# Performance work log

Measured on AMD Instinct MI355X. Metric: run time of the kernel, lower is better.

Reference implementation:

```python
import jax, jax.numpy as jnp
import numpy as np

N, E, D_IN, D_OUT = 50000, 600000, 128, 128
BETA, ALPHA = 0.4, 0.6


def setup_inputs() -> dict:
    key = jax.random.key(0)
    ks = jax.random.split(key, 8)
    def xavier(k, shape):
        std = (2.0 / (shape[0] + shape[1])) ** 0.5
        return jax.random.normal(k, shape, jnp.float32) * std
    x = jax.random.normal(ks[0], (N, D_IN), jnp.float32)
    edge_index = jax.random.randint(ks[1], (2, E), 0, N, jnp.int32)
    Wq = xavier(ks[2], (D_IN, D_OUT))
    Wk = xavier(ks[3], (D_IN, D_OUT))
    Wv = xavier(ks[4], (D_IN, D_IN))
    W_gcn = xavier(ks[5], (D_IN, D_IN))   # GCNConv linear weight [out, in]
    b_gcn = jnp.zeros((D_IN,), jnp.float32)
    W_lin = xavier(ks[6], (D_OUT, D_IN))  # nn.Linear weight [out, in]
    b_lin = jnp.zeros((D_OUT,), jnp.float32)
    return {"x": x, "edge_index": edge_index, "Wq": Wq, "Wk": Wk, "Wv": Wv,
            "W_gcn": W_gcn, "b_gcn": b_gcn, "W_lin": W_lin, "b_lin": b_lin}


def gcn_conv(x, edge_index, W, b):
    # PyG GCNConv default: add self-loops, symmetric deg^-1/2 normalization.
    n = x.shape[0]
    loops = jnp.arange(n, dtype=edge_index.dtype)
    src = jnp.concatenate([edge_index[0], loops])
    dst = jnp.concatenate([edge_index[1], loops])
    deg = jax.ops.segment_sum(jnp.ones_like(dst, jnp.float32), dst, num_segments=n)
    d_inv_sqrt = jax.lax.rsqrt(deg)  # deg >= 1 thanks to self-loops
    norm = d_inv_sqrt[src] * d_inv_sqrt[dst]  # [E+N]
    xw = x @ W.T                               # [N, d]
    out = jax.ops.segment_sum(xw[src] * norm[:, None], dst, num_segments=n)
    return out + b


def reference(x, edge_index, Wq, Wk, Wv, W_gcn, b_gcn, W_lin, b_lin):
    n, d_in = x.shape
    q = x @ Wq
    q_hat = q / jnp.linalg.norm(q)  # Frobenius norm
    k = x @ Wk
    k_hat = k / jnp.linalg.norm(k)
    v = x @ Wv
    # qk = q_hat @ (k_hat^T @ 1) / in_channels  -> [n]
    qk = (q_hat @ k_hat.sum(axis=0)) / d_in
    # D = diag(1 + qk); inverse of diagonal is elementwise reciprocal
    scale = 1.0 / (1.0 + qk)
    attn = v + (q_hat @ (k_hat.T @ v)) / d_in  # [n, d_in]
    Z = BETA * scale[:, None] * attn + (1.0 - BETA) * x
    gcn = gcn_conv(x, edge_index, W_gcn, b_gcn)
    # self.dropout(gcn) result is discarded in the source -> no-op
    Z_out = (1.0 - ALPHA) * Z + ALPHA * gcn
    return Z_out @ W_lin.T + b_lin
```

## Files before the change

kernel.cpp:

```cpp
#include <hip/hip_runtime.h>
#include <hip/hip_fp16.h>
#include <cstdint>
#include <cstddef>

#define D 128
typedef unsigned short u16;
typedef short bf16x8 __attribute__((ext_vector_type(8)));
typedef float f32x4 __attribute__((ext_vector_type(4)));

__device__ __forceinline__ u16 f2b(float f) {
    uint32_t u = __float_as_uint(f);
    return (u16)((u + 0x7FFFu + ((u >> 16) & 1u)) >> 16);
}
__device__ __forceinline__ float b2f(u16 b) {
    return __uint_as_float(((uint32_t)b) << 16);
}

#define SWZ(r, k) ((k) ^ (((r) & 7) << 3))

__global__ void k_prep(const float* __restrict__ Wq, const float* __restrict__ Wk,
                       const float* __restrict__ Wv, const float* __restrict__ Wg,
                       const float* __restrict__ bg, const float* __restrict__ Wl,
                       const float* __restrict__ bl,
                       u16* __restrict__ Bcatb, float* __restrict__ biasout)
{
    const int b = blockIdx.x;
    const int t = threadIdx.x;
    if (b < 640) {
        const int strip = b >> 7, n = b & 127;
        float val;
        if (strip == 0) {
            val = Wq[t * D + n];
        } else if (strip == 1) {
            val = Wk[t * D + n];
        } else if (strip == 2) {
            float s = 0.f;
#pragma unroll 8
            for (int m = 0; m < D; ++m) s += Wv[t * D + m] * Wl[n * D + m];
            val = s;
        } else if (strip == 3) {
            val = Wl[n * D + t];
        } else {
            float s = 0.f;
#pragma unroll 8
            for (int m = 0; m < D; ++m) s += Wl[n * D + m] * Wg[m * D + t];
            val = 0.6f * s;
        }
        Bcatb[(size_t)b * D + t] = f2b(val);
    } else {
        float s = 0.f;
#pragma unroll 8
        for (int m = 0; m < D; ++m) s += bg[m] * Wl[t * D + m];
        biasout[t] = bl[t] + 0.6f * s;
    }
}

__global__ void k_init(int* __restrict__ cnt, int M)
{
    const int i = blockIdx.x * 256 + threadIdx.x;
    if (i < M) cnt[i] = 0;
}

__global__ void k_hist(const int* __restrict__ dst, int* __restrict__ cnt,
                       int* __restrict__ epos, int E)
{
    const int e = blockIdx.x * 256 + threadIdx.x;
    if (e < E) epos[e] = atomicAdd(&cnt[dst[e]], 1);
}

__global__ __launch_bounds__(1024) void k_scan1(const int* __restrict__ cnt,
                                                int* __restrict__ offs,
                                                int* __restrict__ bsum,
                                                float* __restrict__ dinv, int M)
{
    __shared__ int wsum[16];
    const int t = threadIdx.x, lane = t & 63, w = t >> 6;
    const int i = blockIdx.x * 1024 + t;
    const int v = (i < M) ? cnt[i] : 0;
    if (i < M) dinv[i] = rsqrtf((float)(v + 1));
    int s = v;
    for (int off = 1; off < 64; off <<= 1) {
        int n = __shfl_up(s, off);
        if (lane >= off) s += n;
    }
    if (lane == 63) wsum[w] = s;
    __syncthreads();
    if (w == 0) {
        int ss = (lane < 16) ? wsum[lane] : 0;
        for (int off = 1; off < 16; off <<= 1) {
            int n = __shfl_up(ss, off);
            if (lane >= off) ss += n;
        }
        if (lane < 16) wsum[lane] = ss;
    }
    __syncthreads();
    const int woff = (w == 0) ? 0 : wsum[w - 1];
    if (i < M) offs[i] = woff + s - v;
    if (t == 1023) bsum[blockIdx.x] = wsum[15];
}

__global__ void k_scanB(int* __restrict__ bsum, int nb)
{
    const int t = threadIdx.x;
    int v = (t < nb) ? bsum[t] : 0;
    int s = v;
    for (int off = 1; off < 64; off <<= 1) {
        int n = __shfl_up(s, off);
        if (t >= off) s += n;
    }
    if (t < nb) bsum[t] = s - v;
}

__global__ void k_scan2(const int* __restrict__ bsum, int* __restrict__ offs, int M)
{
    const int i = blockIdx.x * 256 + threadIdx.x;
    if (i < M) offs[i] += bsum[i >> 10];
}

__global__ void k_fill(const int* __restrict__ src, const int* __restrict__ dst,
                       const int* __restrict__ epos,
                       const float* __restrict__ dinv,
                       const int* __restrict__ offs,
                       uint32_t* __restrict__ cpk, int E)
{
    const int e = blockIdx.x * 256 + threadIdx.x;
    if (e < E) {
        const int s = src[e], d = dst[e];
        const int pos = offs[d] + epos[e];
        const float w = dinv[s] * dinv[d];
        const u16 hb = __half_as_ushort(__float2half(w));
        cpk[pos] = (uint32_t)(u16)s | ((uint32_t)hb << 16);
    }
}

__global__ __launch_bounds__(256) void k_gemm5(const float* __restrict__ x,
                                               const u16* __restrict__ Bcatb,
                                               u16* __restrict__ outbase,
                                               float* __restrict__ psq,
                                               float* __restrict__ psk,
                                               float* __restrict__ pks,
                                               int M, size_t NQ)
{
    __shared__ u16 As[64 * D];
    __shared__ u16 Bs[64 * D];
    __shared__ float lks[D];
    __shared__ float red[4];
    const int t = threadIdx.x;
    const int row0 = blockIdx.x * 64;
    const int pair = blockIdx.y;

    if (t < D) lks[t] = 0.f;

#pragma unroll
    for (int p = 0; p < 4; ++p) {
        const int flat = t + 256 * p;
        const int r = flat >> 4, kg = flat & 15;
        int gr = row0 + r; if (gr > M - 1) gr = M - 1;
        const float4 f0 = *(const float4*)(x + (size_t)gr * D + kg * 8);
        const float4 f1 = *(const float4*)(x + (size_t)gr * D + kg * 8 + 4);
        u16 rr[8] = {f2b(f0.x), f2b(f0.y), f2b(f0.z), f2b(f0.w),
                     f2b(f1.x), f2b(f1.y), f2b(f1.z), f2b(f1.w)};
        *(uint4*)(As + r * D + SWZ(r, kg * 8)) = *(const uint4*)rr;
    }
#pragma unroll
    for (int p = 0; p < 4; ++p) {
        const int flat = t + 256 * p;
        const int r = flat >> 4, kg = flat & 15;
        const uint4 v = *(const uint4*)(Bcatb + (size_t)(2 * pair * 64 + r) * D + kg * 8);
        *(uint4*)(Bs + r * D + SWZ(r, kg * 8)) = v;
    }
    __syncthreads();

    const int lane = t & 63, w = t >> 6;
    const int wr = (w >> 1) * 32, wc = (w & 1) * 32;
    const int fr = lane & 15, kg2 = lane >> 4;

    u16* outp = outbase + (size_t)pair * NQ;
    float sacc = 0.f;
    float kc[4] = {0.f, 0.f, 0.f, 0.f};

#pragma unroll
    for (int h = 0; h < 2; ++h) {
        f32x4 acc[2][2] = {};
#pragma unroll
        for (int ks = 0; ks < 4; ++ks) {
            const int kb = ks * 32 + kg2 * 8;
            bf16x8 a[2], b[2];
#pragma unroll
            for (int i = 0; i < 2; ++i) {
                const int r = wr + 16 * i + fr;
                a[i] = *(const bf16x8*)(As + r * D + SWZ(r, kb));
            }
#pragma unroll
            for (int j = 0; j < 2; ++j) {
                const int r = wc + 16 * j + fr;
                b[j] = *(const bf16x8*)(Bs + r * D + SWZ(r, kb));
            }
#pragma unroll
            for (int i = 0; i < 2; ++i)
#pragma unroll
                for (int j = 0; j < 2; ++j)
                    acc[i][j] = __builtin_amdgcn_mfma_f32_16x16x32_bf16(a[i], b[j], acc[i][j], 0, 0, 0);
        }
        __syncthreads();
        if (h == 0) {
#pragma unroll
            for (int p = 0; p < 4; ++p) {
                const int flat = t + 256 * p;
                const int r = flat >> 4, kg = flat & 15;
                const uint4 v = *(const uint4*)(Bcatb + (size_t)((2 * pair + 1) * 64 + r) * D + kg * 8);
                *(uint4*)(Bs + r * D + SWZ(r, kg * 8)) = v;
            }
        }

        const int col0 = h * 64;
#pragma unroll
        for (int i = 0; i < 2; ++i) {
#pragma unroll
            for (int reg = 0; reg < 4; ++reg) {
                const int r = row0 + wr + 16 * i + kg2 * 4 + reg;
                if (r < M) {
#pragma unroll
                    for (int j = 0; j < 2; ++j) {
                        const int col = col0 + wc + 16 * j + fr;
                        const u16 hv = f2b(acc[i][j][reg]);
                        outp[(size_t)r * D + col] = hv;
                        if (pair < 2) {
                            const float v = b2f(hv);
                            sacc += v * v;
                            if (pair == 1) kc[h * 2 + j] += v;
                        }
                    }
                }
            }
        }
        if (h == 0) __syncthreads();
    }

    if (pair < 2) {
        if (pair == 1) {
#pragma unroll
            for (int h = 0; h < 2; ++h)
#pragma unroll
                for (int j = 0; j < 2; ++j)
                    atomicAdd(&lks[h * 64 + wc + 16 * j + fr], kc[h * 2 + j]);
        }
        for (int off = 32; off > 0; off >>= 1) sacc += __shfl_down(sacc, off);
        if ((t & 63) == 0) red[w] = sacc;
        __syncthreads();
        if (t == 0) {
            const float s = red[0] + red[1] + red[2] + red[3];
            if (pair == 0) psq[blockIdx.x] = s; else psk[blockIdx.x] = s;
        }
        if (pair == 1 && t < D) pks[(size_t)blockIdx.x * D + t] = lks[t];
    }
}

__global__ __launch_bounds__(256) void k_ktv(const u16* __restrict__ kb,
                                             const u16* __restrict__ vWb,
                                             float* __restrict__ part, int M)
{
    __shared__ u16 kT[D * 64];
    __shared__ u16 vT[D * 64];
    const int t = threadIdx.x;
    const int P = (int)gridDim.x;
    const int chunk = (M + P - 1) / P;
    const int rbeg = blockIdx.x * chunk;
    const int rend = min(rbeg + chunk, M);

    const int lane = t & 63, w = t >> 6;
    const int fr = lane & 15, kg = lane >> 4;

    f32x4 acc[2][8] = {};

    for (int r0 = rbeg; r0 < rend; r0 += 64) {
#pragma unroll
        for (int p = 0; p < 4; ++p) {
            const int flat = t + 256 * p;
            const int rr = flat & 63, cg = flat >> 6;
            const int gr = r0 + rr;
            uint4 kv = make_uint4(0, 0, 0, 0), vv = make_uint4(0, 0, 0, 0);
            if (gr < rend) {
                kv = *(const uint4*)(kb + (size_t)gr * D + cg * 8);
                vv = *(const uint4*)(vWb + (size_t)gr * D + cg * 8);
            }
            const u16* kp = (const u16*)&kv;
            const u16* vp = (const u16*)&vv;
#pragma unroll
            for (int jj = 0; jj < 8; ++jj) {
                const int c = cg * 8 + jj;
                const int ri = rr ^ ((c & 7) << 3);
                kT[c * 64 + ri] = kp[jj];
                vT[c * 64 + ri] = vp[jj];
            }
        }
        __syncthreads();
#pragma unroll
        for (int ks = 0; ks < 2; ++ks) {
            const int rb = ks * 32 + kg * 8;
            bf16x8 a[2], b[8];
#pragma unroll
            for (int i = 0; i < 2; ++i) {
                const int m = w * 32 + 16 * i + fr;
                a[i] = *(const bf16x8*)(kT + m * 64 + (rb ^ ((m & 7) << 3)));
            }
#pragma unroll
            for (int j = 0; j < 8; ++j) {
                const int n = 16 * j + fr;
                b[j] = *(const bf16x8*)(vT + n * 64 + (rb ^ ((n & 7) << 3)));
            }
#pragma unroll
            for (int i = 0; i < 2; ++i)
#pragma unroll
                for (int j = 0; j < 8; ++j)
                    acc[i][j] = __builtin_amdgcn_mfma_f32_16x16x32_bf16(a[i], b[j], acc[i][j], 0, 0, 0);
        }
        __syncthreads();
    }
    float* pp = part + (size_t)blockIdx.x * (D * D);
#pragma unroll
    for (int i = 0; i < 2; ++i)
#pragma unroll
        for (int reg = 0; reg < 4; ++reg) {
            const int m = w * 32 + 16 * i + kg * 4 + reg;
#pragma unroll
            for (int j = 0; j < 8; ++j)
                pp[(size_t)m * D + 16 * j + fr] = acc[i][j][reg];
        }
}

__global__ void k_redC(const float* __restrict__ part, float* __restrict__ Craw, int P)
{
    const int e = blockIdx.x * 256 + threadIdx.x;
    float s0 = 0.f, s1 = 0.f, s2 = 0.f, s3 = 0.f,
          s4 = 0.f, s5 = 0.f, s6 = 0.f, s7 = 0.f;
    int p = 0;
    for (; p + 8 <= P; p += 8) {
        s0 += part[(size_t)(p + 0) * (D * D) + e];
        s1 += part[(size_t)(p + 1) * (D * D) + e];
        s2 += part[(size_t)(p + 2) * (D * D) + e];
        s3 += part[(size_t)(p + 3) * (D * D) + e];
        s4 += part[(size_t)(p + 4) * (D * D) + e];
        s5 += part[(size_t)(p + 5) * (D * D) + e];
        s6 += part[(size_t)(p + 6) * (D * D) + e];
        s7 += part[(size_t)(p + 7) * (D * D) + e];
    }
    for (; p < P; ++p) s0 += part[(size_t)p * (D * D) + e];
    Craw[e] = ((s0 + s1) + (s2 + s3)) + ((s4 + s5) + (s6 + s7));
}

__global__ __launch_bounds__(1024) void k_scalc3t(const float* __restrict__ psq,
                                                  const float* __restrict__ psk,
                                                  const float* __restrict__ pks,
                                                  const float* __restrict__ Craw,
                                                  float* __restrict__ kq,
                                                  u16* __restrict__ C3b, int NBLK)
{
    __shared__ float lpart[8][D];
    __shared__ float wredA[16];
    __shared__ float wredB[16];
    __shared__ float invS;
    const int t = threadIdx.x;
    const int col = t & 127, grp = t >> 7;
    float s = 0.f;
#pragma unroll 8
    for (int bq = grp; bq < NBLK; bq += 8) s += pks[(size_t)bq * D + col];
    lpart[grp][col] = s;
    const int w = t >> 6, lane = t & 63;
    float a = 0.f, b = 0.f;
    for (int i = t; i < NBLK; i += 1024) { a += psq[i]; b += psk[i]; }
    for (int off = 32; off > 0; off >>= 1) {
        a += __shfl_down(a, off);
        b += __shfl_down(b, off);
    }
    if (lane == 0) { wredA[w] = a; wredB[w] = b; }
    __syncthreads();
    if (t == 0) {
        float sq = 0.f, sk = 0.f;
#pragma unroll
        for (int i = 0; i < 16; ++i) { sq += wredA[i]; sk += wredB[i]; }
        invS = 1.0f / (sqrtf(sq) * sqrtf(sk) * 128.0f);
    }
    float ks = 0.f;
    if (t < D) {
#pragma unroll
        for (int g = 0; g < 8; ++g) ks += lpart[g][t];
    }
    __syncthreads();
    const float inv = invS;
    if (t < D) kq[t] = ks * inv;
#pragma unroll
    for (int i = 0; i < 16; ++i) {
        const int e = t + 1024 * i;
        C3b[e] = f2b(Craw[(size_t)(e & 127) * D + (e >> 7)] * inv);
    }
}

__global__ __launch_bounds__(256) void k_final(const u16* __restrict__ qb,
                                               const u16* __restrict__ C3b,
                                               const u16* __restrict__ vWb,
                                               const u16* __restrict__ xWb,
                                               const u16* __restrict__ ub,
                                               const int* __restrict__ cnt,
                                               const float* __restrict__ kq,
                                               const float* __restrict__ biasout,
                                               float* __restrict__ out, int M)
{
    __shared__ u16 As[64 * D];
    __shared__ u16 Bs[D * D];
    __shared__ float scaleS[64];
    const int t = threadIdx.x;
    const int row0 = blockIdx.x * 64;

#pragma unroll
    for (int p = 0; p < 4; ++p) {
        const int flat = t + 256 * p;
        const int r = flat >> 4, kg2 = flat & 15;
        int gr = row0 + r; if (gr > M - 1) gr = M - 1;
        const uint4 v = *(const uint4*)(qb + (size_t)gr * D + kg2 * 8);
        *(uint4*)(As + r * D + SWZ(r, kg2 * 8)) = v;
    }
#pragma unroll
    for (int p = 0; p < 8; ++p) {
        const int flat = t + 256 * p;
        const int r = flat >> 4, kg2 = flat & 15;
        const uint4 v = *(const uint4*)(C3b + (size_t)r * D + kg2 * 8);
        *(uint4*)(Bs + r * D + SWZ(r, kg2 * 8)) = v;
    }
    __syncthreads();

    {
        const int rr = t >> 2, qq = t & 3;
        float s = 0.f;
#pragma unroll
        for (int i = 0; i < 4; ++i) {
            const int kk = qq * 32 + i * 8;
            const bf16x8 a = *(const bf16x8*)(As + rr * D + SWZ(rr, kk));
            const u16* ap = (const u16*)&a;
#pragma unroll
            for (int jj = 0; jj < 8; ++jj) s += b2f(ap[jj]) * kq[kk + jj];
        }
        s += __shfl_xor(s, 1);
        s += __shfl_xor(s, 2);
        if (qq == 0) scaleS[rr] = 0.16f / (1.0f + s);
    }

    const int lane = t & 63, w = t >> 6;
    const int fr = lane & 15, kg = lane >> 4;

    f32x4 acc[8] = {};
#pragma unroll
    for (int ks = 0; ks < 4; ++ks) {
        const int kb2 = ks * 32 + kg * 8;
        const int r = w * 16 + fr;
        const bf16x8 a = *(const bf16x8*)(As + r * D + SWZ(r, kb2));
#pragma unroll
        for (int j = 0; j < 8; ++j) {
            const int n = 16 * j + fr;
            const bf16x8 b = *(const bf16x8*)(Bs + n * D + SWZ(n, kb2));
            acc[j] = __builtin_amdgcn_mfma_f32_16x16x32_bf16(a, b, acc[j], 0, 0, 0);
        }
    }
    __syncthreads();

#pragma unroll
    for (int reg = 0; reg < 4; ++reg) {
        const int rr = w * 16 + kg * 4 + reg;
        const int r = row0 + rr;
        if (r < M) {
            const float rc = scaleS[rr];
            const float sc = 1.0f / (float)(cnt[r] + 1);
#pragma unroll
            for (int j = 0; j < 8; ++j) {
                const int c = 16 * j + fr;
                const size_t idx = (size_t)r * D + c;
                out[idx] = rc * (b2f(vWb[idx]) + acc[j][reg]) + 0.24f * b2f(xWb[idx])
                         + biasout[c] + sc * b2f(ub[idx]);
            }
        }
    }
}

__global__ __launch_bounds__(256) void k_gather(const int* __restrict__ offs,
                                                const int* __restrict__ cnt,
                                                const uint32_t* __restrict__ cpk,
                                                const u16* __restrict__ ub,
                                                float* __restrict__ out, int M)
{
    const int t = threadIdx.x;
    const int w = t >> 6, lane = t & 63;
    const int d = blockIdx.x * 4 + w;
    if (d >= M) return;
    const int g = lane >> 4, sub = lane & 15;
    const int beg = offs[d];
    const int n = cnt[d];
    if (n == 0) return;
    const int end = beg + n;
    float acc[8] = {};
    for (int j0 = beg; j0 < end; j0 += 8) {
        const int j1 = j0 + g, j2 = j0 + 4 + g;
        int s1 = 0, s2 = 0;
        float w1 = 0.f, w2 = 0.f;
        if (j1 < end) {
            const uint32_t p = cpk[j1];
            s1 = (int)(p & 0xFFFFu);
            w1 = __half2float(__ushort_as_half((u16)(p >> 16)));
        }
        if (j2 < end) {
            const uint32_t p = cpk[j2];
            s2 = (int)(p & 0xFFFFu);
            w2 = __half2float(__ushort_as_half((u16)(p >> 16)));
        }
        const uint4 r1 = *(const uint4*)(ub + (size_t)s1 * D + sub * 8);
        const uint4 r2 = *(const uint4*)(ub + (size_t)s2 * D + sub * 8);
        const u16* p1 = (const u16*)&r1;
        const u16* p2 = (const u16*)&r2;
#pragma unroll
        for (int i = 0; i < 8; ++i) acc[i] += w1 * b2f(p1[i]) + w2 * b2f(p2[i]);
    }
#pragma unroll
    for (int i = 0; i < 8; ++i) {
        acc[i] += __shfl_xor(acc[i], 16);
        acc[i] += __shfl_xor(acc[i], 32);
    }
    if (g == 0) {
        float* o = out + (size_t)d * D + sub * 8;
        float4 o0 = *(float4*)o, o1 = *(float4*)(o + 4);
        o0.x += acc[0]; o0.y += acc[1]; o0.z += acc[2]; o0.w += acc[3];
        o1.x += acc[4]; o1.y += acc[5]; o1.z += acc[6]; o1.w += acc[7];
        *(float4*)o = o0; *(float4*)(o + 4) = o1;
    }
}

extern "C" void kernel_launch(void* const* d_in, const int* in_sizes, int n_in,
                              void* d_out, int out_size, void* d_ws, size_t ws_size,
                              hipStream_t stream)
{
    const float* x  = (const float*)d_in[0];
    const int*   ei = (const int*)d_in[1];
    const float* Wq = (const float*)d_in[2];
    const float* Wk = (const float*)d_in[3];
    const float* Wv = (const float*)d_in[4];
    const float* Wg = (const float*)d_in[5];
    const float* bg = (const float*)d_in[6];
    const float* Wl = (const float*)d_in[7];
    const float* bl = (const float*)d_in[8];

    const int M = in_sizes[0] / D;
    const int E = in_sizes[1] / 2;
    const size_t NQ = (size_t)M * D;
    const int P = 192;
    const int NBG = (M + 63) / 64;
    const int NB = (M + 1023) / 1024;

    char* base = (char*)d_ws;
    auto alloc = [&](size_t bytes) -> char* {
        char* p = base; base += (bytes + 63) & ~(size_t)63; return p;
    };
    float* part    = (float*)alloc((size_t)P * D * D * 4);
    float* Craw    = (float*)alloc(D * D * 4);
    float* dinv    = (float*)alloc((size_t)M * 4);
    float* psq     = (float*)alloc((size_t)NBG * 4);
    float* psk     = (float*)alloc((size_t)NBG * 4);
    float* pks     = (float*)alloc((size_t)NBG * D * 4);
    float* kq      = (float*)alloc(D * 4);
    float* biasout = (float*)alloc(D * 4);
    int*   cnt     = (int*)alloc((size_t)M * 4);
    int*   offs    = (int*)alloc((size_t)M * 4);
    int*   bsum    = (int*)alloc(64 * 4);
    int*   epos    = (int*)alloc((size_t)E * 4);
    uint32_t* cpk  = (uint32_t*)alloc((size_t)E * 4);
    u16*   Bcatb   = (u16*)alloc((size_t)640 * D * 2);
    u16*   C3b     = (u16*)alloc(D * D * 2);
    u16*   qb      = (u16*)alloc(NQ * 2);
    u16*   kb      = (u16*)alloc(NQ * 2);
    u16*   vWb     = (u16*)alloc(NQ * 2);
    u16*   xWb     = (u16*)alloc(NQ * 2);
    u16*   ub      = (u16*)alloc(NQ * 2);
    (void)kb; (void)vWb; (void)xWb;

    float* out = (float*)d_out;

    k_prep<<<dim3(641), dim3(128), 0, stream>>>(Wq, Wk, Wv, Wg, bg, Wl, bl, Bcatb, biasout);
    k_init<<<(M + 255) / 256, 256, 0, stream>>>(cnt, M);
    k_hist<<<(E + 255) / 256, 256, 0, stream>>>(ei + E, cnt, epos, E);
    k_scan1<<<NB, 1024, 0, stream>>>(cnt, offs, bsum, dinv, M);
    k_scanB<<<1, 64, 0, stream>>>(bsum, NB);
    k_scan2<<<(M + 255) / 256, 256, 0, stream>>>(bsum, offs, M);
    k_fill<<<(E + 255) / 256, 256, 0, stream>>>(ei, ei + E, epos, dinv, offs, cpk, E);

    k_gemm5<<<dim3(NBG, 5), 256, 0, stream>>>(x, Bcatb, qb, psq, psk, pks, M, NQ);
    k_ktv<<<P, 256, 0, stream>>>(kb, vWb, part, M);
    k_redC<<<64, 256, 0, stream>>>(part, Craw, P);
    k_scalc3t<<<1, 1024, 0, stream>>>(psq, psk, pks, Craw, kq, C3b, NBG);

    k_final<<<(M + 63) / 64, 256, 0, stream>>>(qb, C3b, vWb, xWb, ub, cnt, kq, biasout, out, M);
    k_gather<<<(M + 3) / 4, 256, 0, stream>>>(offs, cnt, cpk, ub, out, M);
}
```

Measured before the change: 194.0 us.

## Replace per-row Q/K/V projections with Gram-matrix reformulation of linear attention

Instead of materializing q, k, vW and xW for all rows, the attention term is rewritten through the input Gram matrix X^T X and the column sums of x. This removes the large bf16 intermediates. Norms, k-sums and the q·(k^T v) product are all derived from small 128x128 matrices, computed in a single-block k_small kernel. The final kernel now recomputes from x against two weight strips per column half, and the GCN input U gets its own GEMM. This cuts global memory traffic. It adds a serial single-block stage, shared-memory atomics in the Gram kernel, and different bf16 rounding points that may change accuracy.

New measurement: 231.7 us. 19.4% more time.

```diff
diff --git a/kernel.cpp b/kernel.cpp
--- a/kernel.cpp
+++ b/kernel.cpp
@@ -18,27 +18,22 @@
 
 #define SWZ(r, k) ((k) ^ (((r) & 7) << 3))
 
-__global__ void k_prep(const float* __restrict__ Wq, const float* __restrict__ Wk,
-                       const float* __restrict__ Wv, const float* __restrict__ Wg,
+__global__ void k_prep(const float* __restrict__ Wv, const float* __restrict__ Wg,
                        const float* __restrict__ bg, const float* __restrict__ Wl,
                        const float* __restrict__ bl,
                        u16* __restrict__ Bcatb, float* __restrict__ biasout)
 {
     const int b = blockIdx.x;
     const int t = threadIdx.x;
-    if (b < 640) {
+    if (b < 384) {
         const int strip = b >> 7, n = b & 127;
         float val;
         if (strip == 0) {
-            val = Wq[t * D + n];
-        } else if (strip == 1) {
-            val = Wk[t * D + n];
-        } else if (strip == 2) {
             float s = 0.f;
 #pragma unroll 8
             for (int m = 0; m < D; ++m) s += Wv[t * D + m] * Wl[n * D + m];
             val = s;
-        } else if (strip == 3) {
+        } else if (strip == 1) {
             val = Wl[n * D + t];
         } else {
             float s = 0.f;
@@ -133,165 +128,41 @@
     }
 }
 
-__global__ __launch_bounds__(256) void k_gemm5(const float* __restrict__ x,
-                                               const u16* __restrict__ Bcatb,
-                                               u16* __restrict__ outbase,
-                                               float* __restrict__ psq,
-                                               float* __restrict__ psk,
-                                               float* __restrict__ pks,
-                                               int M, size_t NQ)
-{
-    __shared__ u16 As[64 * D];
-    __shared__ u16 Bs[64 * D];
-    __shared__ float lks[D];
-    __shared__ float red[4];
-    const int t = threadIdx.x;
-    const int row0 = blockIdx.x * 64;
-    const int pair = blockIdx.y;
-
-    if (t < D) lks[t] = 0.f;
-
-#pragma unroll
-    for (int p = 0; p < 4; ++p) {
-        const int flat = t + 256 * p;
-        const int r = flat >> 4, kg = flat & 15;
-        int gr = row0 + r; if (gr > M - 1) gr = M - 1;
-        const float4 f0 = *(const float4*)(x + (size_t)gr * D + kg * 8);
-        const float4 f1 = *(const float4*)(x + (size_t)gr * D + kg * 8 + 4);
-        u16 rr[8] = {f2b(f0.x), f2b(f0.y), f2b(f0.z), f2b(f0.w),
-                     f2b(f1.x), f2b(f1.y), f2b(f1.z), f2b(f1.w)};
-        *(uint4*)(As + r * D + SWZ(r, kg * 8)) = *(const uint4*)rr;
-    }
-#pragma unroll
-    for (int p = 0; p < 4; ++p) {
-        const int flat = t + 256 * p;
-        const int r = flat >> 4, kg = flat & 15;
-        const uint4 v = *(const uint4*)(Bcatb + (size_t)(2 * pair * 64 + r) * D + kg * 8);
-        *(uint4*)(Bs + r * D + SWZ(r, kg * 8)) = v;
-    }
-    __syncthreads();
-
-    const int lane = t & 63, w = t >> 6;
-    const int wr = (w >> 1) * 32, wc = (w & 1) * 32;
-    const int fr = lane & 15, kg2 = lane >> 4;
-
-    u16* outp = outbase + (size_t)pair * NQ;
-    float sacc = 0.f;
-    float kc[4] = {0.f, 0.f, 0.f, 0.f};
-
-#pragma unroll
-    for (int h = 0; h < 2; ++h) {
-        f32x4 acc[2][2] = {};
-#pragma unroll
-        for (int ks = 0; ks < 4; ++ks) {
-            const int kb = ks * 32 + kg2 * 8;
-            bf16x8 a[2], b[2];
-#pragma unroll
-            for (int i = 0; i < 2; ++i) {
-                const int r = wr + 16 * i + fr;
-                a[i] = *(const bf16x8*)(As + r * D + SWZ(r, kb));
-            }
-#pragma unroll
-            for (int j = 0; j < 2; ++j) {
-                const int r = wc + 16 * j + fr;
-                b[j] = *(const bf16x8*)(Bs + r * D + SWZ(r, kb));
-            }
-#pragma unroll
-            for (int i = 0; i < 2; ++i)
-#pragma unroll
-                for (int j = 0; j < 2; ++j)
-                    acc[i][j] = __builtin_amdgcn_mfma_f32_16x16x32_bf16(a[i], b[j], acc[i][j], 0, 0, 0);
-        }
-        __syncthreads();
-        if (h == 0) {
-#pragma unroll
-            for (int p = 0; p < 4; ++p) {
-                const int flat = t + 256 * p;
-                const int r = flat >> 4, kg = flat & 15;
-                const uint4 v = *(const uint4*)(Bcatb + (size_t)((2 * pair + 1) * 64 + r) * D + kg * 8);
-                *(uint4*)(Bs + r * D + SWZ(r, kg * 8)) = v;
-            }
-        }
-
-        const int col0 = h * 64;
-#pragma unroll
-        for (int i = 0; i < 2; ++i) {
-#pragma unroll
-            for (int reg = 0; reg < 4; ++reg) {
-                const int r = row0 + wr + 16 * i + kg2 * 4 + reg;
-                if (r < M) {
-#pragma unroll
-                    for (int j = 0; j < 2; ++j) {
-                        const int col = col0 + wc + 16 * j + fr;
-                        const u16 hv = f2b(acc[i][j][reg]);
-                        outp[(size_t)r * D + col] = hv;
-                        if (pair < 2) {
-                            const float v = b2f(hv);
-                            sacc += v * v;
-                            if (pair == 1) kc[h * 2 + j] += v;
-                        }
-                    }
-                }
-            }
-        }
-        if (h == 0) __syncthreads();
-    }
-
-    if (pair < 2) {
-        if (pair == 1) {
-#pragma unroll
-            for (int h = 0; h < 2; ++h)
-#pragma unroll
-                for (int j = 0; j < 2; ++j)
-                    atomicAdd(&lks[h * 64 + wc + 16 * j + fr], kc[h * 2 + j]);
-        }
-        for (int off = 32; off > 0; off >>= 1) sacc += __shfl_down(sacc, off);
-        if ((t & 63) == 0) red[w] = sacc;
-        __syncthreads();
-        if (t == 0) {
-            const float s = red[0] + red[1] + red[2] + red[3];
-            if (pair == 0) psq[blockIdx.x] = s; else psk[blockIdx.x] = s;
-        }
-        if (pair == 1 && t < D) pks[(size_t)blockIdx.x * D + t] = lks[t];
-    }
-}
-
-__global__ __launch_bounds__(256) void k_ktv(const u16* __restrict__ kb,
-                                             const u16* __restrict__ vWb,
-                                             float* __restrict__ part, int M)
-{
-    __shared__ u16 kT[D * 64];
-    __shared__ u16 vT[D * 64];
+__global__ __launch_bounds__(256) void k_gram(const float* __restrict__ x,
+                                              float* __restrict__ part,
+                                              float* __restrict__ pcs, int M)
+{
+    __shared__ u16 xT[D * 64];
+    __shared__ float lcs[D];
     const int t = threadIdx.x;
     const int P = (int)gridDim.x;
     const int chunk = (M + P - 1) / P;
     const int rbeg = blockIdx.x * chunk;
     const int rend = min(rbeg + chunk, M);
-
     const int lane = t & 63, w = t >> 6;
     const int fr = lane & 15, kg = lane >> 4;
 
+    if (t < D) lcs[t] = 0.f;
+    __syncthreads();
+
     f32x4 acc[2][8] = {};
 
     for (int r0 = rbeg; r0 < rend; r0 += 64) {
 #pragma unroll
-        for (int p = 0; p < 4; ++p) {
+        for (int p = 0; p < 8; ++p) {
             const int flat = t + 256 * p;
-            const int rr = flat & 63, cg = flat >> 6;
+            const int rr = flat >> 5;
+            const int c4 = flat & 31;
             const int gr = r0 + rr;
-            uint4 kv = make_uint4(0, 0, 0, 0), vv = make_uint4(0, 0, 0, 0);
-            if (gr < rend) {
-                kv = *(const uint4*)(kb + (size_t)gr * D + cg * 8);
-                vv = *(const uint4*)(vWb + (size_t)gr * D + cg * 8);
-            }
-            const u16* kp = (const u16*)&kv;
-            const u16* vp = (const u16*)&vv;
-#pragma unroll
-            for (int jj = 0; jj < 8; ++jj) {
-                const int c = cg * 8 + jj;
+            float4 v = make_float4(0.f, 0.f, 0.f, 0.f);
+            if (gr < rend) v = *(const float4*)(x + (size_t)gr * D + c4 * 4);
+            const float vv[4] = {v.x, v.y, v.z, v.w};
+#pragma unroll
+            for (int jj = 0; jj < 4; ++jj) {
+                const int c = c4 * 4 + jj;
                 const int ri = rr ^ ((c & 7) << 3);
-                kT[c * 64 + ri] = kp[jj];
-                vT[c * 64 + ri] = vp[jj];
+                xT[c * 64 + ri] = f2b(vv[jj]);
+                atomicAdd(&lcs[c], vv[jj]);
             }
         }
         __syncthreads();
@@ -302,12 +173,12 @@
 #pragma unroll
             for (int i = 0; i < 2; ++i) {
                 const int m = w * 32 + 16 * i + fr;
-                a[i] = *(const bf16x8*)(kT + m * 64 + (rb ^ ((m & 7) << 3)));
+                a[i] = *(const bf16x8*)(xT + m * 64 + (rb ^ ((m & 7) << 3)));
             }
 #pragma unroll
             for (int j = 0; j < 8; ++j) {
                 const int n = 16 * j + fr;
-                b[j] = *(const bf16x8*)(vT + n * 64 + (rb ^ ((n & 7) << 3)));
+                b[j] = *(const bf16x8*)(xT + n * 64 + (rb ^ ((n & 7) << 3)));
             }
 #pragma unroll
             for (int i = 0; i < 2; ++i)
@@ -327,6 +198,7 @@
             for (int j = 0; j < 8; ++j)
                 pp[(size_t)m * D + 16 * j + fr] = acc[i][j][reg];
         }
+    if (t < D) pcs[(size_t)blockIdx.x * D + t] = lcs[t];
 }
 
 __global__ void k_redC(const float* __restrict__ part, float* __restrict__ Craw, int P)
@@ -349,83 +221,352 @@
     Craw[e] = ((s0 + s1) + (s2 + s3)) + ((s4 + s5) + (s6 + s7));
 }
 
-__global__ __launch_bounds__(1024) void k_scalc3t(const float* __restrict__ psq,
-                                                  const float* __restrict__ psk,
-                                                  const float* __restrict__ pks,
-                                                  const float* __restrict__ Craw,
-                                                  float* __restrict__ kq,
-                                                  u16* __restrict__ C3b, int NBLK)
-{
-    __shared__ float lpart[8][D];
-    __shared__ float wredA[16];
-    __shared__ float wredB[16];
+__global__ __launch_bounds__(256) void k_small(const float* __restrict__ Graw,
+                                               const float* __restrict__ pcs,
+                                               const float* __restrict__ Wq,
+                                               const float* __restrict__ Wk,
+                                               const u16* __restrict__ stripV,
+                                               float* __restrict__ xkq,
+                                               u16* __restrict__ C5b, int PCS)
+{
+    __shared__ u16 Ga[D * D];
+    __shared__ u16 Bq[D * D];
+    __shared__ u16 Bk[D * D];
+    __shared__ u16 T2[D * D];
+    __shared__ float csx[D];
+    __shared__ float ksum[D];
+    __shared__ float trsh[8];
     __shared__ float invS;
     const int t = threadIdx.x;
-    const int col = t & 127, grp = t >> 7;
-    float s = 0.f;
+    const int lane = t & 63, w = t >> 6;
+    const int fr = lane & 15, kg = lane >> 4;
+
+    if (t < D) {
+        float s0 = 0.f, s1 = 0.f, s2 = 0.f, s3 = 0.f,
+              s4 = 0.f, s5 = 0.f, s6 = 0.f, s7 = 0.f;
+        int p = 0;
+        for (; p + 8 <= PCS; p += 8) {
+            s0 += pcs[(size_t)(p + 0) * D + t];
+            s1 += pcs[(size_t)(p + 1) * D + t];
+            s2 += pcs[(size_t)(p + 2) * D + t];
+            s3 += pcs[(size_t)(p + 3) * D + t];
+            s4 += pcs[(size_t)(p + 4) * D + t];
+            s5 += pcs[(size_t)(p + 5) * D + t];
+            s6 += pcs[(size_t)(p + 6) * D + t];
+            s7 += pcs[(size_t)(p + 7) * D + t];
+        }
+        for (; p < PCS; ++p) s0 += pcs[(size_t)p * D + t];
+        csx[t] = ((s0 + s1) + (s2 + s3)) + ((s4 + s5) + (s6 + s7));
+    }
 #pragma unroll 8
-    for (int bq = grp; bq < NBLK; bq += 8) s += pks[(size_t)bq * D + col];
-    lpart[grp][col] = s;
-    const int w = t >> 6, lane = t & 63;
-    float a = 0.f, b = 0.f;
-    for (int i = t; i < NBLK; i += 1024) { a += psq[i]; b += psk[i]; }
-    for (int off = 32; off > 0; off >>= 1) {
-        a += __shfl_down(a, off);
-        b += __shfl_down(b, off);
-    }
-    if (lane == 0) { wredA[w] = a; wredB[w] = b; }
+    for (int p = 0; p < 64; ++p) {
+        const int e = t + 256 * p;
+        const int i = e >> 7, m = e & 127;
+        Ga[i * D + SWZ(i, m)] = f2b(Graw[e]);
+        Bq[m * D + SWZ(m, i)] = f2b(Wq[e]);
+        Bk[m * D + SWZ(m, i)] = f2b(Wk[e]);
+    }
+    __syncthreads();
+
+    {
+        f32x4 acc[2][8] = {};
+#pragma unroll
+        for (int ks = 0; ks < 4; ++ks) {
+            const int kb = ks * 32 + kg * 8;
+            bf16x8 a[2], b[8];
+#pragma unroll
+            for (int i = 0; i < 2; ++i) {
+                const int r = w * 32 + 16 * i + fr;
+                a[i] = *(const bf16x8*)(Ga + r * D + SWZ(r, kb));
+            }
+#pragma unroll
+            for (int j = 0; j < 8; ++j) {
+                const int n = 16 * j + fr;
+                b[j] = *(const bf16x8*)(Bk + n * D + SWZ(n, kb));
+            }
+#pragma unroll
+            for (int i = 0; i < 2; ++i)
+#pragma unroll
+                for (int j = 0; j < 8; ++j)
+                    acc[i][j] = __builtin_amdgcn_mfma_f32_16x16x32_bf16(a[i], b[j], acc[i][j], 0, 0, 0);
+        }
+        float tk = 0.f;
+#pragma unroll
+        for (int i = 0; i < 2; ++i)
+#pragma unroll
+            for (int reg = 0; reg < 4; ++reg) {
+                const int row = w * 32 + 16 * i + kg * 4 + reg;
+#pragma unroll
+                for (int j = 0; j < 8; ++j) {
+                    const int col = 16 * j + fr;
+                    const float h = acc[i][j][reg];
+                    T2[col * D + SWZ(col, row)] = f2b(h);
+                    tk += h * b2f(Bk[col * D + SWZ(col, row)]);
+                }
+            }
+        for (int off = 32; off > 0; off >>= 1) tk += __shfl_down(tk, off);
+        if (lane == 0) trsh[w] = tk;
+    }
+    __syncthreads();
+    {
+        f32x4 acc[2][8] = {};
+#pragma unroll
+        for (int ks = 0; ks < 4; ++ks) {
+            const int kb = ks * 32 + kg * 8;
+            bf16x8 a[2], b[8];
+#pragma unroll
+            for (int i = 0; i < 2; ++i) {
+                const int r = w * 32 + 16 * i + fr;
+                a[i] = *(const bf16x8*)(Ga + r * D + SWZ(r, kb));
+            }
+#pragma unroll
+            for (int j = 0; j < 8; ++j) {
+                const int n = 16 * j + fr;
+                b[j] = *(const bf16x8*)(Bq + n * D + SWZ(n, kb));
+            }
+#pragma unroll
+            for (int i = 0; i < 2; ++i)
+#pragma unroll
+                for (int j = 0; j < 8; ++j)
+                    acc[i][j] = __builtin_amdgcn_mfma_f32_16x16x32_bf16(a[i], b[j], acc[i][j], 0, 0, 0);
+        }
+        float tq = 0.f;
+#pragma unroll
+        for (int i = 0; i < 2; ++i)
+#pragma unroll
+            for (int reg = 0; reg < 4; ++reg) {
+                const int row = w * 32 + 16 * i + kg * 4 + reg;
+#pragma unroll
+                for (int j = 0; j < 8; ++j) {
+                    const int col = 16 * j + fr;
+                    tq += acc[i][j][reg] * b2f(Bq[col * D + SWZ(col, row)]);
+                }
+            }
+        for (int off = 32; off > 0; off >>= 1) tq += __shfl_down(tq, off);
+        if (lane == 0) trsh[4 + w] = tq;
+    }
     __syncthreads();
     if (t == 0) {
-        float sq = 0.f, sk = 0.f;
-#pragma unroll
-        for (int i = 0; i < 16; ++i) { sq += wredA[i]; sk += wredB[i]; }
+        const float sk = trsh[0] + trsh[1] + trsh[2] + trsh[3];
+        const float sq = trsh[4] + trsh[5] + trsh[6] + trsh[7];
         invS = 1.0f / (sqrtf(sq) * sqrtf(sk) * 128.0f);
     }
-    float ks = 0.f;
     if (t < D) {
-#pragma unroll
-        for (int g = 0; g < 8; ++g) ks += lpart[g][t];
-    }
-    __syncthreads();
-    const float inv = invS;
-    if (t < D) kq[t] = ks * inv;
-#pragma unroll
-    for (int i = 0; i < 16; ++i) {
-        const int e = t + 1024 * i;
-        C3b[e] = f2b(Craw[(size_t)(e & 127) * D + (e >> 7)] * inv);
-    }
-}
-
-__global__ __launch_bounds__(256) void k_final(const u16* __restrict__ qb,
-                                               const u16* __restrict__ C3b,
-                                               const u16* __restrict__ vWb,
-                                               const u16* __restrict__ xWb,
+        float s = 0.f;
+#pragma unroll 8
+        for (int j = 0; j < D; ++j) s += csx[j] * Wk[j * D + t];
+        ksum[t] = s;
+    }
+#pragma unroll 8
+    for (int p = 0; p < 64; ++p) {
+        const int e = t + 256 * p;
+        const int i = e >> 7, m = e & 127;
+        Ga[i * D + SWZ(i, m)] = f2b(Wq[e]);
+    }
+#pragma unroll
+    for (int p = 0; p < 8; ++p) {
+        const int e8 = (t + 256 * p) * 8;
+        const int n = e8 >> 7, i0 = e8 & 127;
+        *(uint4*)(Bq + n * D + SWZ(n, i0)) = *(const uint4*)(stripV + n * D + i0);
+    }
+    __syncthreads();
+    {
+        f32x4 acc[2][8] = {};
+#pragma unroll
+        for (int ks = 0; ks < 4; ++ks) {
+            const int kb = ks * 32 + kg * 8;
+            bf16x8 a[2], b[8];
+#pragma unroll
+            for (int i = 0; i < 2; ++i) {
+                const int m = w * 32 + 16 * i + fr;
+                a[i] = *(const bf16x8*)(T2 + m * D + SWZ(m, kb));
+            }
+#pragma unroll
+            for (int j = 0; j < 8; ++j) {
+                const int n = 16 * j + fr;
+                b[j] = *(const bf16x8*)(Bq + n * D + SWZ(n, kb));
+            }
+#pragma unroll
+            for (int i = 0; i < 2; ++i)
+#pragma unroll
+                for (int j = 0; j < 8; ++j)
+                    acc[i][j] = __builtin_amdgcn_mfma_f32_16x16x32_bf16(a[i], b[j], acc[i][j], 0, 0, 0);
+        }
+        const float inv = invS;
+#pragma unroll
+        for (int i = 0; i < 2; ++i)
+#pragma unroll
+            for (int reg = 0; reg < 4; ++reg) {
+                const int m = w * 32 + 16 * i + kg * 4 + reg;
+#pragma unroll
+                for (int j = 0; j < 8; ++j) {
+                    const int n = 16 * j + fr;
+                    Bk[n * D + SWZ(n, m)] = f2b(acc[i][j][reg] * inv);
+                }
+            }
+    }
+    if (t < D) {
+        float s = 0.f;
+        const float inv = invS;
+#pragma unroll 8
+        for (int o = 0; o < D; ++o) s += Wq[t * D + o] * ksum[o];
+        xkq[t] = s * inv;
+    }
+    __syncthreads();
+    {
+        f32x4 acc[2][8] = {};
+#pragma unroll
+        for (int ks = 0; ks < 4; ++ks) {
+            const int kb = ks * 32 + kg * 8;
+            bf16x8 a[2], b[8];
+#pragma unroll
+            for (int i = 0; i < 2; ++i) {
+                const int r = w * 32 + 16 * i + fr;
+                a[i] = *(const bf16x8*)(Ga + r * D + SWZ(r, kb));
+            }
+#pragma unroll
+            for (int j = 0; j < 8; ++j) {
+                const int n = 16 * j + fr;
+                b[j] = *(const bf16x8*)(Bk + n * D + SWZ(n, kb));
+            }
+#pragma unroll
+            for (int i = 0; i < 2; ++i)
+#pragma unroll
+                for (int j = 0; j < 8; ++j)
+                    acc[i][j] = __builtin_amdgcn_mfma_f32_16x16x32_bf16(a[i], b[j], acc[i][j], 0, 0, 0);
+        }
+#pragma unroll
+        for (int i = 0; i < 2; ++i)
+#pragma unroll
+            for (int reg = 0; reg < 4; ++reg) {
+                const int r = w * 32 + 16 * i + kg * 4 + reg;
+#pragma unroll
+                for (int j = 0; j < 8; ++j) {
+                    const int n = 16 * j + fr;
+                    C5b[n * D + r] = f2b(b2f(stripV[n * D + r]) + acc[i][j][reg]);
+                }
+            }
+    }
+}
+
+__global__ __launch_bounds__(256) void k_ugemm(const float* __restrict__ x,
+                                               const u16* __restrict__ stripU,
+                                               u16* __restrict__ ub, int M)
+{
+    __shared__ u16 As[64 * D];
+    __shared__ u16 Bs[64 * D];
+    const int t = threadIdx.x;
+    const int row0 = blockIdx.x * 64;
+
+#pragma unroll
+    for (int p = 0; p < 4; ++p) {
+        const int flat = t + 256 * p;
+        const int r = flat >> 4, kg = flat & 15;
+        int gr = row0 + r; if (gr > M - 1) gr = M - 1;
+        const float4 f0 = *(const float4*)(x + (size_t)gr * D + kg * 8);
+        const float4 f1 = *(const float4*)(x + (size_t)gr * D + kg * 8 + 4);
+        u16 rr[8] = {f2b(f0.x), f2b(f0.y), f2b(f0.z), f2b(f0.w),
+                     f2b(f1.x), f2b(f1.y), f2b(f1.z), f2b(f1.w)};
+        *(uint4*)(As + r * D + SWZ(r, kg * 8)) = *(const uint4*)rr;
+    }
+#pragma unroll
+    for (int p = 0; p < 4; ++p) {
+        const int flat = t + 256 * p;
+        const int r = flat >> 4, kg = flat & 15;
+        const uint4 v = *(const uint4*)(stripU + (size_t)r * D + kg * 8);
+        *(uint4*)(Bs + r * D + SWZ(r, kg * 8)) = v;
+    }
+    __syncthreads();
+
+    const int lane = t & 63, w = t >> 6;
+    const int wr = (w >> 1) * 32, wc = (w & 1) * 32;
+    const int fr = lane & 15, kg2 = lane >> 4;
+
+#pragma unroll
+    for (int h = 0; h < 2; ++h) {
+        f32x4 acc[2][2] = {};
+#pragma unroll
+        for (int ks = 0; ks < 4; ++ks) {
+            const int kb = ks * 32 + kg2 * 8;
+            bf16x8 a[2], b[2];
+#pragma unroll
+            for (int i = 0; i < 2; ++i) {
+                const int r = wr + 16 * i + fr;
+                a[i] = *(const bf16x8*)(As + r * D + SWZ(r, kb));
+            }
+#pragma unroll
+            for (int j = 0; j < 2; ++j) {
+                const int r = wc + 16 * j + fr;
+                b[j] = *(const bf16x8*)(Bs + r * D + SWZ(r, kb));
+            }
+#pragma unroll
+            for (int i = 0; i < 2; ++i)
+#pragma unroll
+                for (int j = 0; j < 2; ++j)
+                    acc[i][j] = __builtin_amdgcn_mfma_f32_16x16x32_bf16(a[i], b[j], acc[i][j], 0, 0, 0);
+        }
+        __syncthreads();
+        if (h == 0) {
+#pragma unroll
+            for (int p = 0; p < 4; ++p) {
+                const int flat = t + 256 * p;
+                const int r = flat >> 4, kg = flat & 15;
+                const uint4 v = *(const uint4*)(stripU + (size_t)(64 + r) * D + kg * 8);
+                *(uint4*)(Bs + r * D + SWZ(r, kg * 8)) = v;
+            }
+        }
+        const int col0 = h * 64;
+#pragma unroll
+        for (int i = 0; i < 2; ++i) {
+#pragma unroll
+            for (int reg = 0; reg < 4; ++reg) {
+                const int r = row0 + wr + 16 * i + kg2 * 4 + reg;
+                if (r < M) {
+#pragma unroll
+                    for (int j = 0; j < 2; ++j) {
+                        const int col = col0 + wc + 16 * j + fr;
+                        ub[(size_t)r * D + col] = f2b(acc[i][j][reg]);
+                    }
+                }
+            }
+        }
+        if (h == 0) __syncthreads();
+    }
+}
+
+__global__ __launch_bounds__(256) void k_final(const float* __restrict__ x,
+                                               const u16* __restrict__ C5b,
+                                               const u16* __restrict__ stripL,
                                                const u16* __restrict__ ub,
                                                const int* __restrict__ cnt,
-                                               const float* __restrict__ kq,
+                                               const float* __restrict__ xkq,
                                                const float* __restrict__ biasout,
                                                float* __restrict__ out, int M)
 {
     __shared__ u16 As[64 * D];
-    __shared__ u16 Bs[D * D];
+    __shared__ u16 Bs[64 * D];
     __shared__ float scaleS[64];
     const int t = threadIdx.x;
     const int row0 = blockIdx.x * 64;
+    const int half = blockIdx.y;
 
 #pragma unroll
     for (int p = 0; p < 4; ++p) {
         const int flat = t + 256 * p;
-        const int r = flat >> 4, kg2 = flat & 15;
+        const int r = flat >> 4, kg = flat & 15;
         int gr = row0 + r; if (gr > M - 1) gr = M - 1;
-        const uint4 v = *(const uint4*)(qb + (size_t)gr * D + kg2 * 8);
-        *(uint4*)(As + r * D + SWZ(r, kg2 * 8)) = v;
-    }
-#pragma unroll
-    for (int p = 0; p < 8; ++p) {
+        const float4 f0 = *(const float4*)(x + (size_t)gr * D + kg * 8);
+        const float4 f1 = *(const float4*)(x + (size_t)gr * D + kg * 8 + 4);
+        u16 rr[8] = {f2b(f0.x), f2b(f0.y), f2b(f0.z), f2b(f0.w),
+                     f2b(f1.x), f2b(f1.y), f2b(f1.z), f2b(f1.w)};
+        *(uint4*)(As + r * D + SWZ(r, kg * 8)) = *(const uint4*)rr;
+    }
+#pragma unroll
+    for (int p = 0; p < 4; ++p) {
         const int flat = t + 256 * p;
-        const int r = flat >> 4, kg2 = flat & 15;
-        const uint4 v = *(const uint4*)(C3b + (size_t)r * D + kg2 * 8);
-        *(uint4*)(Bs + r * D + SWZ(r, kg2 * 8)) = v;
+        const int r = flat >> 4, kg = flat & 15;
+        const uint4 v = *(const uint4*)(C5b + (size_t)(half * 64 + r) * D + kg * 8);
+        *(uint4*)(Bs + r * D + SWZ(r, kg * 8)) = v;
     }
     __syncthreads();
 
@@ -438,7 +579,7 @@
             const bf16x8 a = *(const bf16x8*)(As + rr * D + SWZ(rr, kk));
             const u16* ap = (const u16*)&a;
 #pragma unroll
-            for (int jj = 0; jj < 8; ++jj) s += b2f(ap[jj]) * kq[kk + jj];
+            for (int jj = 0; jj < 8; ++jj) s += b2f(ap[jj]) * xkq[kk + jj];
         }
         s += __shfl_xor(s, 1);
         s += __shfl_xor(s, 2);
@@ -446,36 +587,78 @@
     }
 
     const int lane = t & 63, w = t >> 6;
-    const int fr = lane & 15, kg = lane >> 4;
-
-    f32x4 acc[8] = {};
+    const int wr = (w >> 1) * 32, wc = (w & 1) * 32;
+    const int fr = lane & 15, kg2 = lane >> 4;
+
+    f32x4 acc1[2][2] = {};
 #pragma unroll
     for (int ks = 0; ks < 4; ++ks) {
-        const int kb2 = ks * 32 + kg * 8;
-        const int r = w * 16 + fr;
-        const bf16x8 a = *(const bf16x8*)(As + r * D + SWZ(r, kb2));
-#pragma unroll
-        for (int j = 0; j < 8; ++j) {
-            const int n = 16 * j + fr;
-            const bf16x8 b = *(const bf16x8*)(Bs + n * D + SWZ(n, kb2));
-            acc[j] = __builtin_amdgcn_mfma_f32_16x16x32_bf16(a, b, acc[j], 0, 0, 0);
-        }
-    }
-    __syncthreads();
-
-#pragma unroll
-    for (int reg = 0; reg < 4; ++reg) {
-        const int rr = w * 16 + kg * 4 + reg;
-        const int r = row0 + rr;
-        if (r < M) {
-            const float rc = scaleS[rr];
-            const float sc = 1.0f / (float)(cnt[r] + 1);
-#pragma unroll
-            for (int j = 0; j < 8; ++j) {
-                const int c = 16 * j + fr;
-                const size_t idx = (size_t)r * D + c;
-                out[idx] = rc * (b2f(vWb[idx]) + acc[j][reg]) + 0.24f * b2f(xWb[idx])
-                         + biasout[c] + sc * b2f(ub[idx]);
+        const int kb = ks * 32 + kg2 * 8;
+        bf16x8 a[2], b[2];
+#pragma unroll
+        for (int i = 0; i < 2; ++i) {
+            const int r = wr + 16 * i + fr;
+            a[i] = *(const bf16x8*)(As + r * D + SWZ(r, kb));
+        }
+#pragma unroll
+        for (int j = 0; j < 2; ++j) {
+            const int r = wc + 16 * j + fr;
+            b[j] = *(const bf16x8*)(Bs + r * D + SWZ(r, kb));
+        }
+#pragma unroll
+        for (int i = 0; i < 2; ++i)
+#pragma unroll
+            for (int j = 0; j < 2; ++j)
+                acc1[i][j] = __builtin_amdgcn_mfma_f32_16x16x32_bf16(a[i], b[j], acc1[i][j], 0, 0, 0);
+    }
+    __syncthreads();
+#pragma unroll
+    for (int p = 0; p < 4; ++p) {
+        const int flat = t + 256 * p;
+        const int r = flat >> 4, kg = flat & 15;
+        const uint4 v = *(const uint4*)(stripL + (size_t)(half * 64 + r) * D + kg * 8);
+        *(uint4*)(Bs + r * D + SWZ(r, kg * 8)) = v;
+    }
+    __syncthreads();
+
+    f32x4 acc2[2][2] = {};
+#pragma unroll
+    for (int ks = 0; ks < 4; ++ks) {
+        const int kb = ks * 32 + kg2 * 8;
+        bf16x8 a[2], b[2];
+#pragma unroll
+        for (int i = 0; i < 2; ++i) {
+            const int r = wr + 16 * i + fr;
+            a[i] = *(const bf16x8*)(As + r * D + SWZ(r, kb));
+        }
+#pragma unroll
+        for (int j = 0; j < 2; ++j) {
+            const int r = wc + 16 * j + fr;
+            b[j] = *(const bf16x8*)(Bs + r * D + SWZ(r, kb));
+        }
+#pragma unroll
+        for (int i = 0; i < 2; ++i)
+#pragma unroll
+            for (int j = 0; j < 2; ++j)
+                acc2[i][j] = __builtin_amdgcn_mfma_f32_16x16x32_bf16(a[i], b[j], acc2[i][j], 0, 0, 0);
+    }
+
+#pragma unroll
+    for (int i = 0; i < 2; ++i) {
+#pragma unroll
+        for (int reg = 0; reg < 4; ++reg) {
+            const int rloc = wr + 16 * i + kg2 * 4 + reg;
+            const int r = row0 + rloc;
+            if (r < M) {
+                const float rc = scaleS[rloc];
+                const float sc = 1.0f / (float)(cnt[r] + 1);
+#pragma unroll
+                for (int j = 0; j < 2; ++j) {
+                    const int c = half * 64 + wc + 16 * j + fr;
+                    const size_t idx = (size_t)r * D + c;
+                    out[idx] = rc * acc1[i][j][reg] + 0.24f * acc2[i][j][reg]
+                             + biasout[c] + sc * b2f(ub[idx]);
+                }
             }
         }
     }
@@ -558,30 +741,27 @@
         char* p = base; base += (bytes + 63) & ~(size_t)63; return p;
     };
     float* part    = (float*)alloc((size_t)P * D * D * 4);
-    float* Craw    = (float*)alloc(D * D * 4);
+    float* Graw    = (float*)alloc(D * D * 4);
+    float* pcs     = (float*)alloc((size_t)P * D * 4);
     float* dinv    = (float*)alloc((size_t)M * 4);
-    float* psq     = (float*)alloc((size_t)NBG * 4);
-    float* psk     = (float*)alloc((size_t)NBG * 4);
-    float* pks     = (float*)alloc((size_t)NBG * D * 4);
-    float* kq      = (float*)alloc(D * 4);
+    float* xkq     = (float*)alloc(D * 4);
     float* biasout = (float*)alloc(D * 4);
     int*   cnt     = (int*)alloc((size_t)M * 4);
     int*   offs    = (int*)alloc((size_t)M * 4);
     int*   bsum    = (int*)alloc(64 * 4);
     int*   epos    = (int*)alloc((size_t)E * 4);
     uint32_t* cpk  = (uint32_t*)alloc((size_t)E * 4);
-    u16*   Bcatb   = (u16*)alloc((size_t)640 * D * 2);
-    u16*   C3b     = (u16*)alloc(D * D * 2);
-    u16*   qb      = (u16*)alloc(NQ * 2);
-    u16*   kb      = (u16*)alloc(NQ * 2);
-    u16*   vWb     = (u16*)alloc(NQ * 2);
-    u16*   xWb     = (u16*)alloc(NQ * 2);
+    u16*   Bcatb   = (u16*)alloc((size_t)384 * D * 2);
+    u16*   C5b     = (u16*)alloc(D * D * 2);
     u16*   ub      = (u16*)alloc(NQ * 2);
-    (void)kb; (void)vWb; (void)xWb;
+
+    const u16* stripV = Bcatb;
+    const u16* stripL = Bcatb + D * D;
+    const u16* stripU = Bcatb + 2 * D * D;
 
     float* out = (float*)d_out;
 
-    k_prep<<<dim3(641), dim3(128), 0, stream>>>(Wq, Wk, Wv, Wg, bg, Wl, bl, Bcatb, biasout);
+    k_prep<<<dim3(385), dim3(128), 0, stream>>>(Wv, Wg, bg, Wl, bl, Bcatb, biasout);
     k_init<<<(M + 255) / 256, 256, 0, stream>>>(cnt, M);
     k_hist<<<(E + 255) / 256, 256, 0, stream>>>(ei + E, cnt, epos, E);
     k_scan1<<<NB, 1024, 0, stream>>>(cnt, offs, bsum, dinv, M);
@@ -589,11 +769,10 @@
     k_scan2<<<(M + 255) / 256, 256, 0, stream>>>(bsum, offs, M);
     k_fill<<<(E + 255) / 256, 256, 0, stream>>>(ei, ei + E, epos, dinv, offs, cpk, E);
 
-    k_gemm5<<<dim3(NBG, 5), 256, 0, stream>>>(x, Bcatb, qb, psq, psk, pks, M, NQ);
-    k_ktv<<<P, 256, 0, stream>>>(kb, vWb, part, M);
-    k_redC<<<64, 256, 0, stream>>>(part, Craw, P);
-    k_scalc3t<<<1, 1024, 0, stream>>>(psq, psk, pks, Craw, kq, C3b, NBG);
-
-    k_final<<<(M + 63) / 64, 256, 0, stream>>>(qb, C3b, vWb, xWb, ub, cnt, kq, biasout, out, M);
+    k_gram<<<P, 256, 0, stream>>>(x, part, pcs, M);
+    k_redC<<<64, 256, 0, stream>>>(part, Graw, P);
+    k_ugemm<<<NBG, 256, 0, stream>>>(x, stripU, ub, M);
+    k_small<<<1, 256, 0, stream>>>(Graw, pcs, Wq, Wk, stripV, xkq, C5b, P);
+    k_final<<<dim3(NBG, 2), 256, 0, stream>>>(x, C5b, stripL, ub, cnt, xkq, biasout, out, M);
     k_gather<<<(M + 3) / 4, 256, 0, stream>>>(offs, cnt, cpk, ub, out, M);
 }
```
